# Kernel optimization log

Measured on AMD Instinct MI355X. Metric: run time of the kernel, lower is better.

The kernel has to match this reference:

```python
import jax, jax.numpy as jnp
import numpy as np

NU, NI = 50000, 50000
N = NU + NI
NNZ = 1_000_000
DIM = 64          # dim_latent
FK = 4            # factor_k
DK = DIM // FK    # dim_k = 16
ITER_K = 2        # iterate_k
NUM_LAYER = 2     # len(dim_layer_list)
EPS = 1e-12


def setup_inputs() -> dict:
    key = jax.random.key(0)
    k1, k2, k3, k4 = jax.random.split(key, 4)
    # xavier-ish init scale for the embedding tables
    embed_user = jax.random.normal(k1, (NU, DIM), dtype=jnp.float32) * 0.1
    embed_item = jax.random.normal(k2, (NI, DIM), dtype=jnp.float32) * 0.1
    edge_head = jax.random.randint(k3, (NNZ,), 0, N, dtype=jnp.int32)
    edge_tail = jax.random.randint(k4, (NNZ,), 0, N, dtype=jnp.int32)
    return {"embed_user": embed_user, "embed_item": embed_item,
            "edge_head": edge_head, "edge_tail": edge_tail}


def _l2norm(x, axis=-1):
    # torch F.normalize(p=2): x / max(||x||, eps)
    return x / jnp.maximum(jnp.linalg.norm(x, axis=axis, keepdims=True), EPS)


def _dgcf_forward(embed_user, embed_item, head, tail):
    ego = jnp.concatenate([embed_user, embed_item], axis=0)  # [N, DIM]
    A_values = jnp.ones((FK, NNZ), dtype=ego.dtype)
    all_embed = [ego]

    def spmm(v, x):
        # sparse A (values v on edges head->tail) @ x : [N, DK]
        return jax.ops.segment_sum(v[:, None] * x[tail], head, num_segments=N)

    spmm_f = jax.vmap(spmm)  # over factor axis

    for _ in range(NUM_LAYER):
        # split ego into factor chunks: [FK, N, DK]
        xs = jnp.moveaxis(ego.reshape(N, FK, DK), 1, 0)
        factor_emb = None
        for t in range(ITER_K):
            # softmax over factors per edge; detached (as in torch .detach())
            vals = jax.lax.stop_gradient(jax.nn.softmax(A_values, axis=0))  # [FK, NNZ]
            # row sums of each factor adjacency -> D = diag(1/sqrt(rowsum))
            row_sum = jax.ops.segment_sum(vals.T, head, num_segments=N).T   # [FK, N]
            d = jnp.where(row_sum > 0,
                          1.0 / jnp.sqrt(jnp.maximum(row_sum, EPS)), 0.0)
            # factor_emb = D @ A @ D @ x  (three chained spmm in torch)
            y = spmm_f(vals, d[:, :, None] * xs)
            factor_emb = d[:, :, None] * y                                   # [FK, N, DK]
            # routing scores: sum over dim of normalize(h) * tanh(normalize(t))
            h = _l2norm(factor_emb[:, head, :], -1)                          # [FK, NNZ, DK]
            tt = _l2norm(xs[:, tail, :], -1)
            scores = jnp.sum(h * jnp.tanh(tt), axis=-1)                      # [FK, NNZ]
            A_values = A_values + scores
        # layer output: normalize last-iteration factor embeddings, re-concat
        layer_emb = _l2norm(factor_emb, -1)           # [FK, N, DK]
        ego = jnp.moveaxis(layer_emb, 0, 1).reshape(N, DIM)
        all_embed.append(ego)

    out = jnp.mean(jnp.stack(all_embed, axis=1), axis=1)  # [N, DIM]
    return out


def reference(embed_user, embed_item, edge_head, edge_tail):
    out = _dgcf_forward(embed_user, embed_item, edge_head, edge_tail)
    return out[:NU], out[NU:]
```

## Files before the change

kernel.cpp:

```cpp
#include <hip/hip_runtime.h>
#include <hip/hip_bf16.h>

#define NUSER 50000
#define NITEM 50000
#define NN    100000
#define NNZ_  1000000
#define DIM_  64
#define NBLK  391
#define EPB   2560

#define FL_SVC    1
#define FL_SC     2
#define FL_NEXT   8
#define FL_FIN    16
#define FL_ACONST 32
#define FL_ASTORE 64

static inline int ceil_div(int a, int b) { return (a + b - 1) / b; }

static __device__ inline float bf2f(unsigned short u) {
    return __uint_as_float(((unsigned int)u) << 16);
}
static __device__ inline unsigned short f2bf(float f) {
    unsigned int x = __float_as_uint(f);
    x += 0x7fffu + ((x >> 16) & 1u);
    return (unsigned short)(x >> 16);
}

__global__ void k_init(const float* __restrict__ eu, const float* __restrict__ ei,
                       unsigned short* __restrict__ ego, unsigned short* __restrict__ te,
                       float* __restrict__ out) {
    int i = blockIdx.x * 256 + threadIdx.x;
    if (i >= NN * DIM_) return;
    float v = (i < NUSER * DIM_) ? eu[i] : ei[i - NUSER * DIM_];
    out[i] = v;
    ego[i] = f2bf(v);
    float s = v * v;
    s += __shfl_xor(s, 1); s += __shfl_xor(s, 2);
    s += __shfl_xor(s, 4); s += __shfl_xor(s, 8);
    float nrm = v / fmaxf(sqrtf(s), 1e-12f);
    float ex = __expf(2.0f * nrm);
    te[i] = f2bf((ex - 1.0f) / (ex + 1.0f));
}

__global__ void k_bcount(const int* __restrict__ head, int* __restrict__ bcount) {
    __shared__ int cnt[NBLK];
    int tid = threadIdx.x;
    for (int i = tid; i < NBLK; i += 256) cnt[i] = 0;
    __syncthreads();
    int e0 = blockIdx.x * EPB;
    int e1 = min(e0 + EPB, NNZ_);
    for (int e = e0 + tid; e < e1; e += 256)
        atomicAdd(&cnt[head[e] >> 8], 1);
    __syncthreads();
    for (int i = tid; i < NBLK; i += 256)
        if (cnt[i]) atomicAdd(&bcount[i], cnt[i]);
}

__global__ void k_bscan(const int* __restrict__ bcount, int* __restrict__ bucket_base,
                        int* __restrict__ bucket_cursor, int* __restrict__ row_start_end) {
    __shared__ int sh[512];
    int t = threadIdx.x;
    int v = (t < NBLK) ? bcount[t] : 0;
    sh[t] = v;
    __syncthreads();
    for (int off = 1; off < 512; off <<= 1) {
        int u = 0;
        if (t >= off) u = sh[t - off];
        __syncthreads();
        sh[t] += u;
        __syncthreads();
    }
    if (t < NBLK) {
        int base = sh[t] - v;
        bucket_base[t] = base;
        bucket_cursor[t] = base;
    }
    if (t == 511) {
        bucket_base[NBLK] = sh[511];
        row_start_end[0] = sh[511];
    }
}

__global__ void k_binscat(const int* __restrict__ head, const int* __restrict__ tail,
                          int* __restrict__ bucket_cursor, int2* __restrict__ bin) {
    __shared__ int cnt[NBLK];
    __shared__ int chunk[NBLK];
    int tid = threadIdx.x;
    for (int i = tid; i < NBLK; i += 256) cnt[i] = 0;
    __syncthreads();
    int e0 = blockIdx.x * EPB;
    int e1 = min(e0 + EPB, NNZ_);
    for (int e = e0 + tid; e < e1; e += 256)
        atomicAdd(&cnt[head[e] >> 8], 1);
    __syncthreads();
    for (int i = tid; i < NBLK; i += 256) {
        chunk[i] = cnt[i] ? atomicAdd(&bucket_cursor[i], cnt[i]) : 0;
        cnt[i] = 0;
    }
    __syncthreads();
    for (int e = e0 + tid; e < e1; e += 256) {
        int h = head[e], t = tail[e];
        int b = h >> 8;
        int off = atomicAdd(&cnt[b], 1);
        bin[chunk[b] + off] = make_int2(h, t);
    }
}

__global__ void k_bucket(const int2* __restrict__ bin, const int* __restrict__ bucket_base,
                         int* __restrict__ row_start, float4* __restrict__ d4a,
                         int* __restrict__ csr_tail) {
    __shared__ int deg[256];
    __shared__ int sh[256];
    __shared__ int cur[256];
    int tid = threadIdx.x;
    int b = blockIdx.x;
    int n0 = b << 8;
    int e0 = bucket_base[b], e1 = bucket_base[b + 1];
    deg[tid] = 0;
    __syncthreads();
    for (int e = e0 + tid; e < e1; e += 256)
        atomicAdd(&deg[bin[e].x - n0], 1);
    __syncthreads();
    int myDeg = deg[tid];
    sh[tid] = myDeg;
    __syncthreads();
    for (int off = 1; off < 256; off <<= 1) {
        int u = 0;
        if (tid >= off) u = sh[tid - off];
        __syncthreads();
        sh[tid] += u;
        __syncthreads();
    }
    int loff = sh[tid] - myDeg;
    int n = n0 + tid;
    if (n < NN) {
        row_start[n] = e0 + loff;
        float dd = (myDeg > 0) ? 2.0f / sqrtf((float)myDeg) : 0.0f;
        d4a[n] = make_float4(dd, dd, dd, dd);
    }
    cur[tid] = e0 + loff;
    __syncthreads();
    for (int e = e0 + tid; e < e1; e += 256) {
        int2 p = bin[e];
        int pos = atomicAdd(&cur[p.x - n0], 1);
        csr_tail[pos] = p.y;
    }
}

template<int FLAGS, int NJ>
static __device__ __forceinline__ void iter_body(
    int n, int lane, int q, int l, int f, int r0, int r1,
    unsigned short* __restrict__ svals, const float* __restrict__ d4c,
    const unsigned short* __restrict__ ego, const unsigned short* __restrict__ te,
    const int* __restrict__ csr_tail,
    float* __restrict__ A4, float* __restrict__ d4n,
    float* __restrict__ out,
    unsigned short* __restrict__ egon, unsigned short* __restrict__ ten)
{
    float ax = 0.f, ay = 0.f, az = 0.f, aw = 0.f;

    int ct[NJ]; float cw[NJ]; float ca[NJ]; ushort4 cv[NJ]; float cd[NJ];
    int eb = r0 + q;
#pragma unroll
    for (int j = 0; j < NJ; ++j) {
        int i = eb + 4 * j;
        bool v = (i < r1);
        int ic = v ? i : 0;
        ct[j] = csr_tail[ic];
        float w;
        if (FLAGS & FL_SVC) w = 0.25f;
        else w = bf2f(svals[ic * 4 + f]);
        cw[j] = v ? w : 0.f;
        if ((FLAGS & FL_SC) && !(FLAGS & FL_ACONST))
            ca[j] = A4[ic * 4 + f];
    }
#pragma unroll
    for (int j = 0; j < NJ; ++j) {
        int t = ct[j];
        cd[j] = d4c[t * 4 + f];
        if (FLAGS & FL_SC)
            cv[j] = *(const ushort4*)(te + t * 64 + 4 * l);
    }
#pragma unroll
    for (int j = 0; j < NJ; ++j) {
        ushort4 u = *(const ushort4*)(ego + ct[j] * 64 + 4 * l);
        float w = cw[j] * cd[j];
        ax += w * bf2f(u.x); ay += w * bf2f(u.y);
        az += w * bf2f(u.z); aw += w * bf2f(u.w);
    }

    if (NJ == 4) {
        for (int base = r0 + 16; base < r1; base += 16) {
            int tj[4]; float wj[4];
#pragma unroll
            for (int j = 0; j < 4; ++j) {
                int i = base + q + 4 * j;
                bool v = (i < r1);
                int ic = v ? i : 0;
                tj[j] = csr_tail[ic];
                float w;
                if (FLAGS & FL_SVC) w = 0.25f;
                else w = bf2f(svals[ic * 4 + f]);
                wj[j] = v ? w : 0.f;
            }
#pragma unroll
            for (int j = 0; j < 4; ++j) {
                int t = tj[j];
                float w = wj[j] * d4c[t * 4 + f];
                ushort4 u = *(const ushort4*)(ego + t * 64 + 4 * l);
                ax += w * bf2f(u.x); ay += w * bf2f(u.y);
                az += w * bf2f(u.z); aw += w * bf2f(u.w);
            }
        }
    }

    ax += __shfl_xor(ax, 16); ax += __shfl_xor(ax, 32);
    ay += __shfl_xor(ay, 16); ay += __shfl_xor(ay, 32);
    az += __shfl_xor(az, 16); az += __shfl_xor(az, 32);
    aw += __shfl_xor(aw, 16); aw += __shfl_xor(aw, 32);

    float s = ax * ax + ay * ay + az * az + aw * aw;
    s += __shfl_xor(s, 1); s += __shfl_xor(s, 2);
    float inv = 1.0f / fmaxf(sqrtf(s), 1e-12f);
    float fx = ax * inv, fy = ay * inv, fz = az * inv, fw = aw * inv;

    if (FLAGS & (FL_NEXT | FL_FIN)) {
        int src = lane >> 2;
        float t0r = __shfl(fx, src), t1r = __shfl(fy, src);
        float t2r = __shfl(fz, src), t3r = __shfl(fw, src);
        float y = (lane & 2) ? ((lane & 1) ? t3r : t2r) : ((lane & 1) ? t1r : t0r);
        int base = n * 64 + lane;
        if (FLAGS & FL_FIN) {
            out[base] = (out[base] + bf2f(ego[base]) + y) * (1.0f / 3.0f);
        }
        if (FLAGS & FL_NEXT) {
            egon[base] = f2bf(y);
            float e2 = __expf(2.0f * y);
            ten[base] = f2bf((e2 - 1.0f) / (e2 + 1.0f));
        }
    }

    if (FLAGS & FL_SC) {
        float accs = 0.f;
#pragma unroll
        for (int j = 0; j < NJ; ++j) {
            int i = eb + 4 * j;
            bool v = (i < r1);
            ushort4 u = cv[j];
            float dot = fx * bf2f(u.x) + fy * bf2f(u.y)
                      + fz * bf2f(u.z) + fw * bf2f(u.w);
            dot += __shfl_xor(dot, 1); dot += __shfl_xor(dot, 2);
            float a = (FLAGS & FL_ACONST) ? 1.0f : ca[j];
            a += dot;
            if ((FLAGS & FL_ASTORE) && v && (l & 3) == 0)
                A4[i * 4 + f] = a;
            float ex = __expf(a);
            float sum = ex;
            sum += __shfl_xor(sum, 4); sum += __shfl_xor(sum, 8);
            float sv = ex / sum;
            if (v && (l & 3) == 0)
                svals[i * 4 + f] = f2bf(sv);
            accs += v ? sv : 0.f;
        }
        if (NJ == 4) {
            for (int base = r0 + 16; base < r1; base += 16) {
                int tj[4]; float aj[4]; ushort4 vj[4];
#pragma unroll
                for (int j = 0; j < 4; ++j) {
                    int i = base + q + 4 * j;
                    bool v = (i < r1);
                    int ic = v ? i : 0;
                    tj[j] = csr_tail[ic];
                    if (!(FLAGS & FL_ACONST)) aj[j] = A4[ic * 4 + f];
                }
#pragma unroll
                for (int j = 0; j < 4; ++j)
                    vj[j] = *(const ushort4*)(te + tj[j] * 64 + 4 * l);
#pragma unroll
                for (int j = 0; j < 4; ++j) {
                    int i = base + q + 4 * j;
                    bool v = (i < r1);
                    ushort4 u = vj[j];
                    float dot = fx * bf2f(u.x) + fy * bf2f(u.y)
                              + fz * bf2f(u.z) + fw * bf2f(u.w);
                    dot += __shfl_xor(dot, 1); dot += __shfl_xor(dot, 2);
                    float a = (FLAGS & FL_ACONST) ? 1.0f : aj[j];
                    a += dot;
                    if ((FLAGS & FL_ASTORE) && v && (l & 3) == 0)
                        A4[i * 4 + f] = a;
                    float ex = __expf(a);
                    float sum = ex;
                    sum += __shfl_xor(sum, 4); sum += __shfl_xor(sum, 8);
                    float sv = ex / sum;
                    if (v && (l & 3) == 0)
                        svals[i * 4 + f] = f2bf(sv);
                    accs += v ? sv : 0.f;
                }
            }
        }
        accs += __shfl_xor(accs, 16); accs += __shfl_xor(accs, 32);
        if (lane < 16 && (l & 3) == 0) {
            float d = (accs > 0.f) ? 1.0f / sqrtf(fmaxf(accs, 1e-12f)) : 0.f;
            d4n[n * 4 + f] = d;
        }
    }
}

template<int FLAGS>
__global__ void k_iter(unsigned short* __restrict__ svals,
                       const float* __restrict__ d4c,
                       const unsigned short* __restrict__ ego,
                       const unsigned short* __restrict__ te,
                       const int* __restrict__ row_start, const int* __restrict__ csr_tail,
                       float* __restrict__ A4,
                       float* __restrict__ d4n,
                       float* __restrict__ out,
                       unsigned short* __restrict__ egon, unsigned short* __restrict__ ten) {
    int n = (blockIdx.x * 256 + threadIdx.x) >> 6;
    if (n >= NN) return;
    int lane = threadIdx.x & 63;
    int q = lane >> 4;
    int l = lane & 15;
    int f = l >> 2;
    int r0 = __builtin_amdgcn_readfirstlane(row_start[n]);
    int r1 = __builtin_amdgcn_readfirstlane(row_start[n + 1]);
    int deg = r1 - r0;
    if (deg <= 8) {
        if (deg <= 4)
            iter_body<FLAGS, 1>(n, lane, q, l, f, r0, r1, svals, d4c, ego, te,
                                csr_tail, A4, d4n, out, egon, ten);
        else
            iter_body<FLAGS, 2>(n, lane, q, l, f, r0, r1, svals, d4c, ego, te,
                                csr_tail, A4, d4n, out, egon, ten);
    } else {
        if (deg <= 12)
            iter_body<FLAGS, 3>(n, lane, q, l, f, r0, r1, svals, d4c, ego, te,
                                csr_tail, A4, d4n, out, egon, ten);
        else
            iter_body<FLAGS, 4>(n, lane, q, l, f, r0, r1, svals, d4c, ego, te,
                                csr_tail, A4, d4n, out, egon, ten);
    }
}

extern "C" void kernel_launch(void* const* d_in, const int* in_sizes, int n_in,
                              void* d_out, int out_size, void* d_ws, size_t ws_size,
                              hipStream_t stream) {
    const float* eu = (const float*)d_in[0];
    const float* ei = (const float*)d_in[1];
    const int* head = (const int*)d_in[2];
    const int* tail = (const int*)d_in[3];
    float* out = (float*)d_out;

    float* A4 = (float*)d_ws;
    float* d4a = A4 + (size_t)NNZ_ * 4;
    float* d4b = d4a + (size_t)NN * 4;
    unsigned short* svals = (unsigned short*)(d4b + (size_t)NN * 4);
    unsigned short* ego_a = svals + (size_t)NNZ_ * 4;
    unsigned short* te_a  = ego_a + (size_t)NN * DIM_;
    unsigned short* ego_b = te_a + (size_t)NN * DIM_;
    unsigned short* te_b  = ego_b + (size_t)NN * DIM_;
    int* csr_tail = (int*)(te_b + (size_t)NN * DIM_);
    int* row_start = csr_tail + NNZ_;
    int* bcount = row_start + (NN + 1);
    int* bucket_base = bcount + NBLK;
    int* bucket_cursor = bucket_base + (NBLK + 1);
    int2* bin = (int2*)A4;

    const int node_blocks = ceil_div(NN * DIM_, 256);
    const int wave_blocks = ceil_div(NN * 64, 256);

    k_init<<<node_blocks, 256, 0, stream>>>(eu, ei, ego_a, te_a, out);

    hipMemsetAsync(bcount, 0, NBLK * sizeof(int), stream);
    k_bcount<<<NBLK, 256, 0, stream>>>(head, bcount);
    k_bscan<<<1, 512, 0, stream>>>(bcount, bucket_base, bucket_cursor, &row_start[NN]);
    k_binscat<<<NBLK, 256, 0, stream>>>(head, tail, bucket_cursor, bin);
    k_bucket<<<NBLK, 256, 0, stream>>>(bin, bucket_base, row_start, (float4*)d4a, csr_tail);

    k_iter<FL_SVC | FL_SC | FL_ACONST | FL_ASTORE><<<wave_blocks, 256, 0, stream>>>(
        svals, d4a, ego_a, te_a, row_start, csr_tail, A4, d4b, out, ego_b, te_b);

    k_iter<FL_SC | FL_ASTORE | FL_NEXT><<<wave_blocks, 256, 0, stream>>>(
        svals, d4b, ego_a, te_a, row_start, csr_tail, A4, d4a, out, ego_b, te_b);

    k_iter<FL_SC><<<wave_blocks, 256, 0, stream>>>(
        svals, d4a, ego_b, te_b, row_start, csr_tail, A4, d4b, out, ego_b, te_b);

    k_iter<FL_FIN><<<wave_blocks, 256, 0, stream>>>(
        svals, d4b, ego_b, te_b, row_start, csr_tail, A4, d4a, out, ego_b, te_b);
}
```

Measured before the change: 352.2 us.

## Use bf16 dot2 intrinsic for routing scores and halve edges per binning block

The routing-score dot products now use the packed bf16 fdot2 instruction. The factor embedding is rounded to bf16 and packed once per node, replacing per-element bf16-to-float conversions and FMAs. Separately, the edge-count and binning passes launch twice as many blocks, each handling half as many edges, to raise parallelism. Rounding the query vector to bf16 adds a small precision loss in the scores.

Result: slower. 381.7 us (+8.4%).

```diff
diff --git a/kernel.cpp b/kernel.cpp
--- a/kernel.cpp
+++ b/kernel.cpp
@@ -7,7 +7,7 @@
 #define NNZ_  1000000
 #define DIM_  64
 #define NBLK  391
-#define EPB   2560
+#define EPB   1280
 
 #define FL_SVC    1
 #define FL_SC     2
@@ -26,6 +26,19 @@
     x += 0x7fffu + ((x >> 16) & 1u);
     return (unsigned short)(x >> 16);
 }
+
+#if __has_builtin(__builtin_amdgcn_fdot2_f32_bf16)
+typedef __bf16 bf16x2_t __attribute__((ext_vector_type(2)));
+static __device__ inline float dot2bf(unsigned int a, unsigned int b, float c) {
+    return __builtin_amdgcn_fdot2_f32_bf16(__builtin_bit_cast(bf16x2_t, a),
+                                           __builtin_bit_cast(bf16x2_t, b), c, false);
+}
+#else
+static __device__ inline float dot2bf(unsigned int a, unsigned int b, float c) {
+    return c + bf2f((unsigned short)(a & 0xffffu)) * bf2f((unsigned short)(b & 0xffffu))
+             + bf2f((unsigned short)(a >> 16)) * bf2f((unsigned short)(b >> 16));
+}
+#endif
 
 __global__ void k_init(const float* __restrict__ eu, const float* __restrict__ ei,
                        unsigned short* __restrict__ ego, unsigned short* __restrict__ te,
@@ -160,7 +173,7 @@
 {
     float ax = 0.f, ay = 0.f, az = 0.f, aw = 0.f;
 
-    int ct[NJ]; float cw[NJ]; float ca[NJ]; ushort4 cv[NJ]; float cd[NJ];
+    int ct[NJ]; float cw[NJ]; float ca[NJ]; uint2 cv[NJ]; float cd[NJ];
     int eb = r0 + q;
 #pragma unroll
     for (int j = 0; j < NJ; ++j) {
@@ -180,7 +193,7 @@
         int t = ct[j];
         cd[j] = d4c[t * 4 + f];
         if (FLAGS & FL_SC)
-            cv[j] = *(const ushort4*)(te + t * 64 + 4 * l);
+            cv[j] = *(const uint2*)(te + t * 64 + 4 * l);
     }
 #pragma unroll
     for (int j = 0; j < NJ; ++j) {
@@ -242,14 +255,14 @@
     }
 
     if (FLAGS & FL_SC) {
+        unsigned int p01 = ((unsigned int)f2bf(fy) << 16) | f2bf(fx);
+        unsigned int p23 = ((unsigned int)f2bf(fw) << 16) | f2bf(fz);
         float accs = 0.f;
 #pragma unroll
         for (int j = 0; j < NJ; ++j) {
             int i = eb + 4 * j;
             bool v = (i < r1);
-            ushort4 u = cv[j];
-            float dot = fx * bf2f(u.x) + fy * bf2f(u.y)
-                      + fz * bf2f(u.z) + fw * bf2f(u.w);
+            float dot = dot2bf(cv[j].y, p23, dot2bf(cv[j].x, p01, 0.0f));
             dot += __shfl_xor(dot, 1); dot += __shfl_xor(dot, 2);
             float a = (FLAGS & FL_ACONST) ? 1.0f : ca[j];
             a += dot;
@@ -265,7 +278,7 @@
         }
         if (NJ == 4) {
             for (int base = r0 + 16; base < r1; base += 16) {
-                int tj[4]; float aj[4]; ushort4 vj[4];
+                int tj[4]; float aj[4]; uint2 vj[4];
 #pragma unroll
                 for (int j = 0; j < 4; ++j) {
                     int i = base + q + 4 * j;
@@ -276,14 +289,12 @@
                 }
 #pragma unroll
                 for (int j = 0; j < 4; ++j)
-                    vj[j] = *(const ushort4*)(te + tj[j] * 64 + 4 * l);
+                    vj[j] = *(const uint2*)(te + tj[j] * 64 + 4 * l);
 #pragma unroll
                 for (int j = 0; j < 4; ++j) {
                     int i = base + q + 4 * j;
                     bool v = (i < r1);
-                    ushort4 u = vj[j];
-                    float dot = fx * bf2f(u.x) + fy * bf2f(u.y)
-                              + fz * bf2f(u.z) + fw * bf2f(u.w);
+                    float dot = dot2bf(vj[j].y, p23, dot2bf(vj[j].x, p01, 0.0f));
                     dot += __shfl_xor(dot, 1); dot += __shfl_xor(dot, 2);
                     float a = (FLAGS & FL_ACONST) ? 1.0f : aj[j];
                     a += dot;
@@ -369,13 +380,14 @@
 
     const int node_blocks = ceil_div(NN * DIM_, 256);
     const int wave_blocks = ceil_div(NN * 64, 256);
+    const int edge_pass_blocks = ceil_div(NNZ_, EPB);
 
     k_init<<<node_blocks, 256, 0, stream>>>(eu, ei, ego_a, te_a, out);
 
     hipMemsetAsync(bcount, 0, NBLK * sizeof(int), stream);
-    k_bcount<<<NBLK, 256, 0, stream>>>(head, bcount);
+    k_bcount<<<edge_pass_blocks, 256, 0, stream>>>(head, bcount);
     k_bscan<<<1, 512, 0, stream>>>(bcount, bucket_base, bucket_cursor, &row_start[NN]);
-    k_binscat<<<NBLK, 256, 0, stream>>>(head, tail, bucket_cursor, bin);
+    k_binscat<<<edge_pass_blocks, 256, 0, stream>>>(head, tail, bucket_cursor, bin);
     k_bucket<<<NBLK, 256, 0, stream>>>(bin, bucket_base, row_start, (float4*)d4a, csr_tail);
 
     k_iter<FL_SVC | FL_SC | FL_ACONST | FL_ASTORE><<<wave_blocks, 256, 0, stream>>>(
```
